# Optimization experiments

Hardware: AMD Instinct MI355X
Metric: run time of the kernel (lower is better)

The kernel has to match this reference:

```python
import jax, jax.numpy as jnp
import numpy as np

EMBED_DIM = 128
NUM_SYMBOLS = 200000
PAD_IDX = NUM_SYMBOLS
K_NEIGHBORS = 10
PROCESS_STEPS = 4
D_MODEL = 2 * EMBED_DIM   # 256
D_INNER = 2 * D_MODEL     # 512
LSTM_HID = 2 * D_MODEL    # 512
B, F_SUP, MAX_K = 4096, 5, 64


def setup_inputs() -> dict:
    key = jax.random.key(0)
    ks = jax.random.split(key, 40)
    f = lambda i, shape, s=0.05: jax.random.normal(ks[i], shape, jnp.float32) * s
    inp = {}
    inp['query'] = jax.random.randint(ks[0], (B, 2), 0, NUM_SYMBOLS)
    inp['support'] = jax.random.randint(ks[1], (F_SUP, 2), 0, NUM_SYMBOLS)
    inp['q_l1'] = jax.random.randint(ks[2], (B, MAX_K, 2), 0, NUM_SYMBOLS + 1)
    inp['q_deg_l'] = jax.random.randint(ks[3], (B,), 0, 100)
    inp['q_r1'] = jax.random.randint(ks[4], (B, MAX_K, 2), 0, NUM_SYMBOLS + 1)
    inp['q_deg_r'] = jax.random.randint(ks[5], (B,), 0, 100)
    inp['s_l1'] = jax.random.randint(ks[6], (F_SUP, MAX_K, 2), 0, NUM_SYMBOLS + 1)
    inp['s_deg_l'] = jax.random.randint(ks[7], (F_SUP,), 0, 100)
    inp['s_r1'] = jax.random.randint(ks[8], (F_SUP, MAX_K, 2), 0, NUM_SYMBOLS + 1)
    inp['s_deg_r'] = jax.random.randint(ks[9], (F_SUP,), 0, 100)
    # learned parameters
    inp['symbol_emb'] = f(10, (NUM_SYMBOLS + 1, EMBED_DIM), 0.1).at[PAD_IDX].set(0.0)
    inp['gcn_w_w'] = f(11, (EMBED_DIM, 2 * EMBED_DIM))
    inp['gcn_w_b'] = jnp.zeros((EMBED_DIM,), jnp.float32)
    inp['gcn_b'] = jnp.zeros((EMBED_DIM,), jnp.float32)
    inp['g1_w'] = f(12, (EMBED_DIM // 2, EMBED_DIM))
    inp['g1_b'] = jnp.zeros((EMBED_DIM // 2,), jnp.float32)
    inp['ln1_g'] = jnp.ones((EMBED_DIM // 2,), jnp.float32)
    inp['ln1_b'] = jnp.zeros((EMBED_DIM // 2,), jnp.float32)
    inp['g2_w'] = f(13, (1, EMBED_DIM // 2))
    inp['g2_b'] = jnp.zeros((1,), jnp.float32)
    inp['gate_temp'] = jnp.array(1.0, jnp.float32)
    inp['se_p1_w'] = f(14, (D_INNER, D_MODEL))
    inp['se_p1_b'] = jnp.zeros((D_INNER,), jnp.float32)
    inp['se_p2_w'] = f(15, (D_MODEL, D_INNER))
    inp['se_p2_b'] = jnp.zeros((D_MODEL,), jnp.float32)
    inp['se_ln_g'] = jnp.ones((D_MODEL,), jnp.float32)
    inp['se_ln_b'] = jnp.zeros((D_MODEL,), jnp.float32)
    inp['w_ih'] = f(16, (4 * LSTM_HID, D_MODEL))
    inp['w_hh'] = f(17, (4 * LSTM_HID, LSTM_HID))
    inp['b_ih'] = jnp.zeros((4 * LSTM_HID,), jnp.float32)
    inp['b_hh'] = jnp.zeros((4 * LSTM_HID,), jnp.float32)
    return inp


def _layernorm(x, g, b, eps=1e-5):
    m = jnp.mean(x, axis=-1, keepdims=True)
    v = jnp.var(x, axis=-1, keepdims=True)
    return (x - m) / jnp.sqrt(v + eps) * g + b


def _l2norm(x):
    return x / jnp.maximum(jnp.linalg.norm(x, axis=-1, keepdims=True), 1e-12)


def _neighbor_encoder(conn, deg, self_ids, p):
    emb = p['symbol_emb']
    rel, ent = conn[:, :, 0], conn[:, :, 1]
    rel_emb = emb[rel]            # [n, K, D] gather
    ent_emb = emb[ent]            # [n, K, D]
    self_emb = emb[self_ids]      # [n, D]
    sim = jnp.einsum('nd,nkd->nk', _l2norm(self_emb), _l2norm(ent_emb))
    is_pad = (rel == PAD_IDX).astype(jnp.float32)
    sim = sim - is_pad * 1e9
    k = min(K_NEIGHBORS, conn.shape[1])
    _, k_idx = jax.lax.top_k(sim, k)
    bidx = jnp.arange(conn.shape[0])[:, None]
    k_mask = jnp.zeros(sim.shape, jnp.float32).at[bidx, k_idx].set(1.0)[..., None]
    concat = jnp.concatenate([rel_emb, ent_emb], axis=-1)   # [n, K, 2D]
    proj = jax.nn.leaky_relu(concat @ p['gcn_w_w'].T + p['gcn_w_b'] + p['gcn_b'], 0.01)
    valid = (1.0 - is_pad[..., None]) * k_mask
    denom = jnp.maximum(jnp.sum(valid, axis=1), 1.0)
    agg = jnp.sum((proj * k_mask) * valid, axis=1) / denom   # [n, D]
    h = jax.nn.relu(_layernorm(agg @ p['g1_w'].T + p['g1_b'], p['ln1_g'], p['ln1_b']))
    logit = h @ p['g2_w'].T + p['g2_b']                      # [n, 1]
    temp = jnp.clip(p['gate_temp'], 0.1, 5.0)
    gate = jax.nn.sigmoid(logit / temp) * (deg > 0).astype(jnp.float32)[:, None]
    return jnp.tanh(self_emb + gate * agg)


def _support_encoder(x, p):
    h = jax.nn.relu(x @ p['se_p1_w'].T + p['se_p1_b'])
    h = h @ p['se_p2_w'].T + p['se_p2_b']
    return _layernorm(h + x, p['se_ln_g'], p['se_ln_b'])


def _query_encoder(support, query, p):
    n = query.shape[0]
    h_r0 = jnp.zeros((n, LSTM_HID), jnp.float32)
    c0 = jnp.zeros((n, LSTM_HID), jnp.float32)

    def step(carry, _):
        h_r, c = carry
        gates = query @ p['w_ih'].T + p['b_ih'] + h_r @ p['w_hh'].T + p['b_hh']
        i, f, g, o = jnp.split(gates, 4, axis=-1)
        c = jax.nn.sigmoid(f) * c + jax.nn.sigmoid(i) * jnp.tanh(g)
        h_ = jax.nn.sigmoid(o) * jnp.tanh(c)
        h = query + h_[:, :D_MODEL]
        attn = jax.nn.softmax(h @ support.T, axis=1)
        r = attn @ support
        return (jnp.concatenate([h, r], axis=-1), c), None

    (h_r, _), _ = jax.lax.scan(step, (h_r0, c0), None, length=PROCESS_STEPS)
    return h_r[:, :D_MODEL]


def reference(query, support, q_l1, q_deg_l, q_r1, q_deg_r, s_l1, s_deg_l, s_r1, s_deg_r,
              symbol_emb, gcn_w_w, gcn_w_b, gcn_b, g1_w, g1_b, ln1_g, ln1_b, g2_w, g2_b,
              gate_temp, se_p1_w, se_p1_b, se_p2_w, se_p2_b, se_ln_g, se_ln_b,
              w_ih, w_hh, b_ih, b_hh):
    p = dict(symbol_emb=symbol_emb, gcn_w_w=gcn_w_w, gcn_w_b=gcn_w_b, gcn_b=gcn_b,
             g1_w=g1_w, g1_b=g1_b, ln1_g=ln1_g, ln1_b=ln1_b, g2_w=g2_w, g2_b=g2_b,
             gate_temp=gate_temp, se_p1_w=se_p1_w, se_p1_b=se_p1_b, se_p2_w=se_p2_w,
             se_p2_b=se_p2_b, se_ln_g=se_ln_g, se_ln_b=se_ln_b,
             w_ih=w_ih, w_hh=w_hh, b_ih=b_ih, b_hh=b_hh)
    q_left = _neighbor_encoder(q_l1, q_deg_l, query[:, 0], p)
    q_right = _neighbor_encoder(q_r1, q_deg_r, query[:, 1], p)
    query_vec = jnp.concatenate([q_left, q_right], axis=-1)      # [B, 2D]
    s_left = _neighbor_encoder(s_l1, s_deg_l, support[:, 0], p)
    s_right = _neighbor_encoder(s_r1, s_deg_r, support[:, 1], p)
    support_vec = jnp.concatenate([s_left, s_right], axis=-1)    # [F, 2D]
    support_g = jnp.mean(_support_encoder(support_vec, p), axis=0, keepdims=True)  # [1, 2D]
    query_enc = _support_encoder(query_vec, p)                   # [B, 2D]
    query_g = _query_encoder(support_g, query_enc, p)            # [B, 2D]
    return jnp.sum(query_g * support_g, axis=1)                  # [B]
```

## Files before the change

kernel.cpp:

```cpp
#include <hip/hip_runtime.h>
#include <math.h>

#define BQ 4096
#define F_SUP 5
#define MAXK 64
#define ED 128
#define DM 256
#define DI 512
#define LH 512
#define NG 2048
#define PADX 200000
#define KNB 10
#define MROWS 82048
#define MREAL 82020
#define MQ 4224
#define EMB_ELEMS 25600128

typedef unsigned short u16;
typedef __attribute__((ext_vector_type(8))) short short8;
typedef __attribute__((ext_vector_type(4))) float floatx4;

__device__ __forceinline__ float sigf(float x) { return 1.0f / (1.0f + __expf(-x)); }
__device__ __forceinline__ float tanh_fast(float x) {
  float a = fabsf(x);
  float e = __expf(-2.0f * a);
  float t = (1.0f - e) / (1.0f + e);
  return copysignf(t, x);
}
__device__ __forceinline__ u16 f2bf(float f) {
  unsigned u = __float_as_uint(f);
  unsigned r = (u + 0x7FFFu + ((u >> 16) & 1u)) >> 16;
  return (u16)r;
}
__device__ __forceinline__ float bf2f(u16 u) {
  return __uint_as_float(((unsigned)u) << 16);
}
__device__ __forceinline__ void gl2lds16(const void* g, void* l) {
  __builtin_amdgcn_global_load_lds(
      (const __attribute__((address_space(1))) void*)g,
      (__attribute__((address_space(3))) void*)l, 16, 0, 0);
}

__global__ __launch_bounds__(256) void emb_cast_kernel(
    const float* __restrict__ emb, u16* __restrict__ embb)
{
  long i = ((long)blockIdx.x * 256 + threadIdx.x) * 8;
  if (i >= (long)EMB_ELEMS) return;
  float4 f0 = *(const float4*)(emb + i);
  float4 f1 = *(const float4*)(emb + i + 4);
  short8 s;
  s[0]=(short)f2bf(f0.x); s[1]=(short)f2bf(f0.y); s[2]=(short)f2bf(f0.z); s[3]=(short)f2bf(f0.w);
  s[4]=(short)f2bf(f1.x); s[5]=(short)f2bf(f1.y); s[6]=(short)f2bf(f1.z); s[7]=(short)f2bf(f1.w);
  *(short8*)(embb + i) = s;
}

__global__ __launch_bounds__(256) void nbr_simrank_kernel(
    const int* __restrict__ query, const int* __restrict__ support,
    const int* __restrict__ q_l1, const int* __restrict__ q_r1,
    const int* __restrict__ s_l1, const int* __restrict__ s_r1,
    const u16* __restrict__ embb, int* __restrict__ idxA, int* __restrict__ meta)
{
  __shared__ float sE[128];
  __shared__ float simS[64];
  __shared__ int relS[64], entS[64];
  int tid = threadIdx.x;
  int b = blockIdx.x;
  const int* conn; int self_id;
  if (b < BQ)              { int i = b;              conn = q_l1 + (long)i*(MAXK*2); self_id = query[2*i];   }
  else if (b < 2*BQ)       { int i = b - BQ;         conn = q_r1 + (long)i*(MAXK*2); self_id = query[2*i+1]; }
  else if (b < 2*BQ+F_SUP) { int i = b - 2*BQ;       conn = s_l1 + (long)i*(MAXK*2); self_id = support[2*i]; }
  else                     { int i = b - 2*BQ-F_SUP; conn = s_r1 + (long)i*(MAXK*2); self_id = support[2*i+1]; }

  int k = tid >> 2, part = tid & 3;
  int2 rc = *(const int2*)(conn + 2 * k);
  if (tid < 16) {
    short8 s = *(const short8*)(embb + (long)self_id * ED + tid * 8);
    #pragma unroll
    for (int j = 0; j < 8; ++j) sE[tid * 8 + j] = bf2f((u16)s[j]);
  }
  __syncthreads();

  const u16* er = embb + (long)rc.y * ED + part * 8;
  float dot = 0.f, sq = 0.f;
  #pragma unroll
  for (int i = 0; i < 4; ++i) {
    short8 e8 = *(const short8*)(er + i * 32);
    #pragma unroll
    for (int j = 0; j < 8; ++j) {
      float e = bf2f((u16)e8[j]);
      float s = sE[i * 32 + part * 8 + j];
      dot += e * s; sq += e * e;
    }
  }
  dot += __shfl_xor(dot, 1); dot += __shfl_xor(dot, 2);
  sq  += __shfl_xor(sq, 1);  sq  += __shfl_xor(sq, 2);
  if (part == 0) {
    float ne = fmaxf(sqrtf(sq), 1e-12f);
    float sim = dot / ne;
    if (rc.x == PADX) sim -= 1e9f;
    simS[k] = sim; relS[k] = rc.x; entS[k] = rc.y;
  }
  __syncthreads();

  if (tid < 64) {
    float my = simS[tid];
    int rank = 0;
    #pragma unroll
    for (int j = 0; j < 64; ++j) {
      float s = simS[j];
      rank += ((s > my) || (s == my && j < tid)) ? 1 : 0;
    }
    bool val = (rank < KNB) && (relS[tid] != PADX);
    unsigned long long vm = __ballot(val ? 1 : 0);
    int cnt = __popcll(vm);
    long base = (long)b * 10;
    if (val) {
      int pos = __popcll(vm & ((1ull << tid) - 1ull));
      int2 p; p.x = relS[tid]; p.y = entS[tid];
      *(int2*)(idxA + (base + pos) * 2) = p;
    }
    if (tid >= cnt && tid < KNB) {
      int2 pp; pp.x = PADX; pp.y = PADX;
      *(int2*)(idxA + (base + tid) * 2) = pp;
    }
    if (tid == 0) meta[b] = cnt;
  }
  if (b == 0 && tid >= 64 && tid < 64 + 2 * (MROWS - MREAL)) {
    idxA[(long)MREAL * 2 + (tid - 64)] = PADX;
  }
}

__global__ __launch_bounds__(256) void proj_gather_gemm(
    const int* __restrict__ idxA, const u16* __restrict__ embb,
    const u16* __restrict__ W, u16* __restrict__ proj)
{
  __shared__ u16 As[128 * 32];
  __shared__ u16 Bs[128 * 32];
  __shared__ int idxS[256];
  int tid = threadIdx.x;
  int bm = blockIdx.x;
  idxS[tid] = idxA[bm * 256 + tid];
  int lane = tid & 63, wave = tid >> 6;
  int wm = (wave & 1) * 64, wn = (wave >> 1) * 64;
  int col = lane & 15, quad = lane >> 4;

  floatx4 acc[4][4];
  #pragma unroll
  for (int i = 0; i < 4; ++i)
    #pragma unroll
    for (int j = 0; j < 4; ++j) { floatx4 z = {0.f,0.f,0.f,0.f}; acc[i][j] = z; }
  __syncthreads();

  for (int k0 = 0; k0 < 256; k0 += 32) {
    int half = k0 >> 7, koff = k0 & 127;
    #pragma unroll
    for (int t = 0; t < 2; ++t) {
      int c = t * 256 + tid;
      int rb = c >> 2, o = c & 3;
      int og = o ^ (rb & 3);
      gl2lds16(W + (long)rb * 256 + k0 + og * 8, &Bs[(size_t)c * 8]);
      int id = idxS[rb * 2 + half];
      gl2lds16(embb + (long)id * ED + koff + og * 8, &As[(size_t)c * 8]);
    }
    __syncthreads();
    short8 af[4], bfr[4];
    #pragma unroll
    for (int i = 0; i < 4; ++i) {
      int ra = wm + i * 16 + col;
      af[i] = *(const short8*)&As[(size_t)(ra * 4 + (quad ^ (ra & 3))) * 8];
      int rb = wn + i * 16 + col;
      bfr[i] = *(const short8*)&Bs[(size_t)(rb * 4 + (quad ^ (rb & 3))) * 8];
    }
    #pragma unroll
    for (int i = 0; i < 4; ++i)
      #pragma unroll
      for (int j = 0; j < 4; ++j)
        acc[i][j] = __builtin_amdgcn_mfma_f32_16x16x32_bf16(af[i], bfr[j], acc[i][j], 0, 0, 0);
    __syncthreads();
  }
  int gm0 = bm * 128 + wm + quad * 4;
  int gn0 = wn + col;
  #pragma unroll
  for (int i = 0; i < 4; ++i)
    #pragma unroll
    for (int j = 0; j < 4; ++j)
      #pragma unroll
      for (int rr = 0; rr < 4; ++rr)
        proj[(long)(gm0 + i * 16 + rr) * 128 + gn0 + j * 16] = f2bf(acc[i][j][rr]);
}

__global__ __launch_bounds__(128) void nbr_post_kernel(
    const int* __restrict__ query, const int* __restrict__ support,
    const int* __restrict__ q_deg_l, const int* __restrict__ q_deg_r,
    const int* __restrict__ s_deg_l, const int* __restrict__ s_deg_r,
    const float* __restrict__ emb,
    const u16* __restrict__ proj, const int* __restrict__ meta,
    const float* __restrict__ gcn_w_b, const float* __restrict__ gcn_b,
    const float* __restrict__ g1_w, const float* __restrict__ g1_b,
    const float* __restrict__ ln1_g, const float* __restrict__ ln1_b,
    const float* __restrict__ g2_w, const float* __restrict__ g2_b,
    const float* __restrict__ gate_temp,
    float* __restrict__ qv, u16* __restrict__ qv_bf)
{
  __shared__ __align__(16) float aggS[128];
  __shared__ float sEs[128];
  __shared__ float gateS;
  int tid = threadIdx.x, b = blockIdx.x;
  int deg, self_id, row, colb;
  if (b < BQ)              { int i = b;              deg = q_deg_l[i]; self_id = query[2*i];     row = i;        colb = 0;  }
  else if (b < 2*BQ)       { int i = b - BQ;         deg = q_deg_r[i]; self_id = query[2*i+1];   row = i;        colb = ED; }
  else if (b < 2*BQ+F_SUP) { int i = b - 2*BQ;       deg = s_deg_l[i]; self_id = support[2*i];   row = BQ + i;   colb = 0;  }
  else                     { int i = b - 2*BQ-F_SUP; deg = s_deg_r[i]; self_id = support[2*i+1]; row = BQ + i;   colb = ED; }
  float* outp = qv + (long)row * DM + colb;
  u16*  outpb = qv_bf + (long)row * DM + colb;

  int cnt = meta[b];
  float denom = fmaxf((float)cnt, 1.0f);
  float bsum = gcn_w_b[tid] + gcn_b[tid];
  float agg = 0.f;
  long pbase = (long)b * 10;
  for (int kk = 0; kk < cnt; ++kk) {
    float z = bf2f(proj[(pbase + kk) * 128 + tid]) + bsum;
    z = (z >= 0.f) ? z : 0.01f * z;
    agg += z;
  }
  agg /= denom;
  aggS[tid] = agg;
  sEs[tid] = emb[(long)self_id * ED + tid];
  __syncthreads();

  if (tid < 64) {
    int e = tid;
    const float4* g1r = (const float4*)(g1_w + e * ED);
    float y = g1_b[e];
    #pragma unroll 8
    for (int j = 0; j < 32; ++j) {
      float4 w = g1r[j];
      float4 a = *(const float4*)&aggS[j * 4];
      y += w.x*a.x + w.y*a.y + w.z*a.z + w.w*a.w;
    }
    float s = y;
    #pragma unroll
    for (int off = 1; off < 64; off <<= 1) s += __shfl_xor(s, off);
    float mean = s * (1.0f / 64.0f);
    float dv = y - mean;
    float s2 = dv * dv;
    #pragma unroll
    for (int off = 1; off < 64; off <<= 1) s2 += __shfl_xor(s2, off);
    float var = s2 * (1.0f / 64.0f);
    float hv = dv / sqrtf(var + 1e-5f) * ln1_g[e] + ln1_b[e];
    hv = fmaxf(hv, 0.f);
    float lp = hv * g2_w[e];
    #pragma unroll
    for (int off = 1; off < 64; off <<= 1) lp += __shfl_xor(lp, off);
    if (e == 0) {
      float logit = lp + g2_b[0];
      float temp = fminf(fmaxf(gate_temp[0], 0.1f), 5.0f);
      float gate = 1.0f / (1.0f + expf(-logit / temp));
      if (deg <= 0) gate = 0.f;
      gateS = gate;
    }
  }
  __syncthreads();
  float o = tanhf(sEs[tid] + gateS * aggS[tid]);
  outp[tid] = o;
  outpb[tid] = f2bf(o);
}

__global__ __launch_bounds__(256) void mfma_gemm(
    const u16* __restrict__ A, int lda,
    const u16* __restrict__ W, int ldw,
    int N, int K,
    float* __restrict__ Cout, u16* __restrict__ Cbf,
    const float* __restrict__ bias0,
    const u16* __restrict__ gqin,
    u16* __restrict__ gqout,
    int relu, int lstm_mode,
    float* __restrict__ cstate, const float* __restrict__ qe,
    u16* __restrict__ hbf)
{
  __shared__ u16 As[128 * 32];
  __shared__ u16 Bs[128 * 32];
  int tid = threadIdx.x;
  int nb = N >> 7;
  int bn = blockIdx.x % nb, bm = blockIdx.x / nb;
  int lane = tid & 63, wave = tid >> 6;
  int wm = (wave & 1) * 64, wn = (wave >> 1) * 64;
  int col = lane & 15, quad = lane >> 4;

  u16 gqa[64]; float cpv[16]; float qev[16]; float scv[4];
  int u = 0; long fb = 0;
  if (lstm_mode) {
    u = bn * 32 + (wave >> 1) * 16 + col;
    fb = ((long)blockIdx.x * 4 + wave) * 64 + lane;
    #pragma unroll
    for (int j = 0; j < 4; ++j)
      scv[j] = bias0[bn * 128 + (wave >> 1) * 64 + j * 16 + col];
    if (lstm_mode == 1) {
      const short8* gp = (const short8*)(gqin + fb * 64);
      #pragma unroll
      for (int t = 0; t < 8; ++t) *(short8*)&gqa[t * 8] = gp[t];
      const float4* cp = (const float4*)(cstate + fb * 16);
      #pragma unroll
      for (int t = 0; t < 4; ++t) *(float4*)&cpv[t * 4] = cp[t];
    }
    if (u < DM) {
      #pragma unroll
      for (int i = 0; i < 4; ++i)
        #pragma unroll
        for (int r = 0; r < 4; ++r) {
          int m = bm * 128 + (wave & 1) * 64 + i * 16 + quad * 4 + r;
          qev[i * 4 + r] = qe[(long)m * DM + u];
        }
    }
  }

  floatx4 acc[4][4];
  #pragma unroll
  for (int i = 0; i < 4; ++i)
    #pragma unroll
    for (int j = 0; j < 4; ++j) { floatx4 z = {0.f,0.f,0.f,0.f}; acc[i][j] = z; }

  for (int k0 = 0; k0 < K; k0 += 32) {
    #pragma unroll
    for (int t = 0; t < 2; ++t) {
      int c = t * 256 + tid;
      int r = c >> 2, o = c & 3;
      int og = o ^ (r & 3);
      gl2lds16(A + (long)(bm * 128 + r) * lda + k0 + og * 8, &As[(size_t)c * 8]);
      gl2lds16(W + (long)(bn * 128 + r) * ldw + k0 + og * 8, &Bs[(size_t)c * 8]);
    }
    __syncthreads();
    short8 af[4], bfr[4];
    #pragma unroll
    for (int i = 0; i < 4; ++i) {
      int ra = wm + i * 16 + col;
      af[i] = *(const short8*)&As[(size_t)(ra * 4 + (quad ^ (ra & 3))) * 8];
      int rb = wn + i * 16 + col;
      bfr[i] = *(const short8*)&Bs[(size_t)(rb * 4 + (quad ^ (rb & 3))) * 8];
    }
    #pragma unroll
    for (int i = 0; i < 4; ++i)
      #pragma unroll
      for (int j = 0; j < 4; ++j)
        acc[i][j] = __builtin_amdgcn_mfma_f32_16x16x32_bf16(af[i], bfr[j], acc[i][j], 0, 0, 0);
    __syncthreads();
  }

  if (lstm_mode) {
    float cnew[16];
    #pragma unroll
    for (int i = 0; i < 4; ++i) {
      #pragma unroll
      for (int r = 0; r < 4; ++r) {
        float gI = acc[i][0][r] + scv[0];
        float gF = acc[i][1][r] + scv[1];
        float gG = acc[i][2][r] + scv[2];
        float gO = acc[i][3][r] + scv[3];
        if (lstm_mode == 1) {
          gI += bf2f(gqa[(i * 4 + 0) * 4 + r]);
          gF += bf2f(gqa[(i * 4 + 1) * 4 + r]);
          gG += bf2f(gqa[(i * 4 + 2) * 4 + r]);
          gO += bf2f(gqa[(i * 4 + 3) * 4 + r]);
        }
        float cp = (lstm_mode == 2) ? 0.f : cpv[i * 4 + r];
        float cn = sigf(gF) * cp + sigf(gI) * tanh_fast(gG);
        cnew[i * 4 + r] = cn;
        if (u < DM) {
          int m = bm * 128 + (wave & 1) * 64 + i * 16 + quad * 4 + r;
          hbf[(long)m * DM + u] = f2bf(qev[i * 4 + r] + sigf(gO) * tanh_fast(cn));
        }
      }
    }
    {
      float4* cp = (float4*)(cstate + fb * 16);
      #pragma unroll
      for (int t = 0; t < 4; ++t) cp[t] = *(float4*)&cnew[t * 4];
    }
    if (lstm_mode == 2) {
      u16 ga[64];
      #pragma unroll
      for (int i = 0; i < 4; ++i)
        #pragma unroll
        for (int j = 0; j < 4; ++j)
          #pragma unroll
          for (int r = 0; r < 4; ++r)
            ga[(i * 4 + j) * 4 + r] = f2bf(acc[i][j][r] + scv[j]);
      short8* gp = (short8*)(gqout + fb * 64);
      #pragma unroll
      for (int t = 0; t < 8; ++t) gp[t] = *(short8*)&ga[t * 8];
    }
  } else {
    int gm0 = bm * 128 + wm + quad * 4;
    int gn0 = bn * 128 + wn + col;
    #pragma unroll
    for (int i = 0; i < 4; ++i) {
      #pragma unroll
      for (int j = 0; j < 4; ++j) {
        int n = gn0 + j * 16;
        #pragma unroll
        for (int r = 0; r < 4; ++r) {
          int m = gm0 + i * 16 + r;
          float v = acc[i][j][r];
          if (bias0) v += bias0[n];
          if (relu) v = fmaxf(v, 0.f);
          if (Cout) Cout[(long)m * N + n] = v;
          if (Cbf)  Cbf[(long)m * N + n] = f2bf(v);
        }
      }
    }
  }
}

__global__ void prep_cast(
    const float* __restrict__ p1, const float* __restrict__ p2,
    const float* __restrict__ gcnw, const float* __restrict__ wih,
    const float* __restrict__ whh, const float* __restrict__ bih,
    const float* __restrict__ bhh,
    u16* __restrict__ p1b, u16* __restrict__ p2b, u16* __restrict__ gcnb,
    u16* __restrict__ wihb, u16* __restrict__ whhb, float* __restrict__ bihh)
{
  int gid = blockIdx.x * 256 + threadIdx.x;
  if (gid < 131072) { p1b[gid] = f2bf(p1[gid]); }
  else if (gid < 262144) { int i = gid - 131072; p2b[i] = f2bf(p2[i]); }
  else if (gid < 294912) { int i = gid - 262144; gcnb[i] = f2bf(gcnw[i]); }
  else if (gid < 819200) {
    int i = gid - 294912; int p = i >> 8, k = i & 255;
    int g = (p >> 4) & 3, uu = (p >> 7) * 32 + ((p >> 6) & 1) * 16 + (p & 15);
    int n = g * 512 + uu;
    wihb[i] = f2bf(wih[(long)n * DM + k]);
  } else if (gid < 1343488) {
    int i = gid - 819200; int p = i >> 8, k = i & 255;
    int g = (p >> 4) & 3, uu = (p >> 7) * 32 + ((p >> 6) & 1) * 16 + (p & 15);
    int n = g * 512 + uu;
    whhb[i] = f2bf(whh[(long)n * LH + k]);
  } else if (gid < 1345536) {
    int p = gid - 1343488;
    int g = (p >> 4) & 3, uu = (p >> 7) * 32 + ((p >> 6) & 1) * 16 + (p & 15);
    int n = g * 512 + uu;
    bihh[p] = bih[n] + bhh[n];
  }
}

__global__ __launch_bounds__(256) void ln_residual_kernel(
    const float* __restrict__ h2buf, const float* __restrict__ xbuf,
    const float* __restrict__ lng, const float* __restrict__ lnb,
    float* __restrict__ out, u16* __restrict__ outb)
{
  __shared__ float red[4];
  int r = blockIdx.x, tid = threadIdx.x;
  float v = h2buf[(long)r * DM + tid] + xbuf[(long)r * DM + tid];
  float s = v;
  #pragma unroll
  for (int off = 1; off < 64; off <<= 1) s += __shfl_xor(s, off);
  if ((tid & 63) == 0) red[tid >> 6] = s;
  __syncthreads();
  float mean = (red[0] + red[1] + red[2] + red[3]) * (1.0f / 256.0f);
  __syncthreads();
  float dv = v - mean;
  float s2 = dv * dv;
  #pragma unroll
  for (int off = 1; off < 64; off <<= 1) s2 += __shfl_xor(s2, off);
  if ((tid & 63) == 0) red[tid >> 6] = s2;
  __syncthreads();
  float var = (red[0] + red[1] + red[2] + red[3]) * (1.0f / 256.0f);
  float o = dv / sqrtf(var + 1e-5f) * lng[tid] + lnb[tid];
  out[(long)r * DM + tid] = o;
  outb[(long)r * DM + tid] = f2bf(o);
}

__global__ __launch_bounds__(256) void scorr_kernel(
    const float* __restrict__ qe, const float* __restrict__ whh,
    float* __restrict__ sg, float* __restrict__ s_corr_perm)
{
  __shared__ float sgS[DM];
  int tid = threadIdx.x;
  {
    float v = 0.f;
    #pragma unroll
    for (int r = 0; r < F_SUP; ++r) v += qe[(long)(BQ + r) * DM + tid];
    v *= (1.0f / (float)F_SUP);
    sgS[tid] = v;
    if (blockIdx.x == 0) sg[tid] = v;
  }
  __syncthreads();
  int wave = tid >> 6, lane = tid & 63;
  int n = blockIdx.x * 4 + wave;
  float4 w = *(const float4*)(whh + (long)n * LH + DM + lane * 4);
  float4 s = *(const float4*)&sgS[lane * 4];
  float d = w.x*s.x + w.y*s.y + w.z*s.z + w.w*s.w;
  #pragma unroll
  for (int off = 1; off < 64; off <<= 1) d += __shfl_xor(d, off);
  if (lane == 0) {
    int g = n >> 9, uu = n & 511;
    int p = (uu >> 5) * 128 + ((uu >> 4) & 1) * 64 + g * 16 + (uu & 15);
    s_corr_perm[p] = d;
  }
}

__global__ __launch_bounds__(256) void final_dot_kernel(
    const u16* __restrict__ h, const float* __restrict__ sg, float* __restrict__ out)
{
  __shared__ float red[4];
  int m = blockIdx.x, tid = threadIdx.x;
  float v = bf2f(h[(long)m * DM + tid]) * sg[tid];
  #pragma unroll
  for (int off = 1; off < 64; off <<= 1) v += __shfl_xor(v, off);
  if ((tid & 63) == 0) red[tid >> 6] = v;
  __syncthreads();
  if (tid == 0) out[m] = red[0] + red[1] + red[2] + red[3];
}

extern "C" void kernel_launch(void* const* d_in, const int* in_sizes, int n_in,
                              void* d_out, int out_size, void* d_ws, size_t ws_size,
                              hipStream_t stream)
{
  const int*   query    = (const int*)  d_in[0];
  const int*   support  = (const int*)  d_in[1];
  const int*   q_l1     = (const int*)  d_in[2];
  const int*   q_deg_l  = (const int*)  d_in[3];
  const int*   q_r1     = (const int*)  d_in[4];
  const int*   q_deg_r  = (const int*)  d_in[5];
  const int*   s_l1     = (const int*)  d_in[6];
  const int*   s_deg_l  = (const int*)  d_in[7];
  const int*   s_r1     = (const int*)  d_in[8];
  const int*   s_deg_r  = (const int*)  d_in[9];
  const float* symbol_emb = (const float*)d_in[10];
  const float* gcn_w_w  = (const float*)d_in[11];
  const float* gcn_w_b  = (const float*)d_in[12];
  const float* gcn_b    = (const float*)d_in[13];
  const float* g1_w     = (const float*)d_in[14];
  const float* g1_b     = (const float*)d_in[15];
  const float* ln1_g    = (const float*)d_in[16];
  const float* ln1_b    = (const float*)d_in[17];
  const float* g2_w     = (const float*)d_in[18];
  const float* g2_b     = (const float*)d_in[19];
  const float* gate_temp= (const float*)d_in[20];
  const float* se_p1_w  = (const float*)d_in[21];
  const float* se_p1_b  = (const float*)d_in[22];
  const float* se_p2_w  = (const float*)d_in[23];
  const float* se_p2_b  = (const float*)d_in[24];
  const float* se_ln_g  = (const float*)d_in[25];
  const float* se_ln_b  = (const float*)d_in[26];
  const float* w_ih     = (const float*)d_in[27];
  const float* w_hh     = (const float*)d_in[28];
  const float* b_ih     = (const float*)d_in[29];
  const float* b_hh     = (const float*)d_in[30];

  float* ws = (float*)d_ws;
  size_t off = 0;
  float* projF   = ws + off; off += (size_t)MROWS * 128 / 2;
  float* idxF    = ws + off; off += (size_t)MROWS * 2;
  float* qv      = ws + off; off += (size_t)MQ * DM;
  float* qe      = ws + off; off += (size_t)MQ * DM;
  float* qv_bfF  = ws + off; off += (size_t)MQ * DM / 2;
  float* qe_bfF  = ws + off; off += (size_t)MQ * DM / 2;
  float* h1bF    = ws + off; off += (size_t)MQ * DI / 2;
  float* H2      = ws + off; off += (size_t)MQ * DM;
  float* gqbF    = ws + off; off += (size_t)BQ * NG / 2;
  float* cstate  = ws + off; off += (size_t)BQ * LH;
  float* hbf0F   = ws + off; off += (size_t)BQ * DM / 2;
  float* hbf1F   = ws + off; off += (size_t)BQ * DM / 2;
  float* p1bF    = ws + off; off += 131072 / 2;
  float* p2bF    = ws + off; off += 131072 / 2;
  float* gcnbF   = ws + off; off += 32768 / 2;
  float* wihbF   = ws + off; off += 524288 / 2;
  float* whhbF   = ws + off; off += 524288 / 2;
  float* bihh    = ws + off; off += 2048;
  float* sg      = ws + off; off += 256;
  float* s_corr  = ws + off; off += 2048;
  float* metaF   = ws + off; off += 8448;
  float* embbF   = ws + off; off += (size_t)EMB_ELEMS / 2;

  u16* proj   = (u16*)projF;
  int* idxA   = (int*)idxF;
  u16* qv_bf  = (u16*)qv_bfF;
  u16* qe_bf  = (u16*)qe_bfF;
  u16* H1_bf  = (u16*)h1bF;
  u16* gq_fr  = (u16*)gqbF;
  u16* hbf0   = (u16*)hbf0F;
  u16* hbf1   = (u16*)hbf1F;
  u16* p1b    = (u16*)p1bF;
  u16* p2b    = (u16*)p2bF;
  u16* gcnb   = (u16*)gcnbF;
  u16* wihb   = (u16*)wihbF;
  u16* whhb   = (u16*)whhbF;
  int* meta   = (int*)metaF;
  u16* embb   = (u16*)embbF;

  prep_cast<<<5256, 256, 0, stream>>>(se_p1_w, se_p2_w, gcn_w_w, w_ih, w_hh, b_ih, b_hh,
                                      p1b, p2b, gcnb, wihb, whhb, bihh);
  emb_cast_kernel<<<(EMB_ELEMS / 8 + 255) / 256, 256, 0, stream>>>(symbol_emb, embb);

  nbr_simrank_kernel<<<2 * BQ + 2 * F_SUP, 256, 0, stream>>>(
      query, support, q_l1, q_r1, s_l1, s_r1, embb, idxA, meta);

  proj_gather_gemm<<<MROWS / 128, 256, 0, stream>>>(idxA, embb, gcnb, proj);

  nbr_post_kernel<<<2 * BQ + 2 * F_SUP, 128, 0, stream>>>(
      query, support, q_deg_l, q_deg_r, s_deg_l, s_deg_r, symbol_emb,
      proj, meta, gcn_w_b, gcn_b, g1_w, g1_b, ln1_g, ln1_b, g2_w, g2_b, gate_temp,
      qv, qv_bf);

  mfma_gemm<<<(MQ / 128) * (DI / 128), 256, 0, stream>>>(qv_bf, 256, p1b, 256, DI, 256,
      nullptr, H1_bf, se_p1_b, nullptr, nullptr, 1, 0, nullptr, nullptr, nullptr);
  mfma_gemm<<<(MQ / 128) * (DM / 128), 256, 0, stream>>>(H1_bf, 512, p2b, 512, DM, 512,
      H2, nullptr, se_p2_b, nullptr, nullptr, 0, 0, nullptr, nullptr, nullptr);
  ln_residual_kernel<<<BQ + F_SUP, 256, 0, stream>>>(H2, qv, se_ln_g, se_ln_b, qe, qe_bf);

  scorr_kernel<<<512, 256, 0, stream>>>(qe, w_hh, sg, s_corr);

  mfma_gemm<<<(BQ / 128) * (NG / 128), 256, 0, stream>>>(qe_bf, 256, wihb, 256, NG, 256,
      nullptr, nullptr, bihh, nullptr, gq_fr, 0, 2, cstate, qe, hbf0);

  mfma_gemm<<<(BQ / 128) * (NG / 128), 256, 0, stream>>>(hbf0, 256, whhb, 256, NG, 256,
      nullptr, nullptr, s_corr, gq_fr, nullptr, 0, 1, cstate, qe, hbf1);
  mfma_gemm<<<(BQ / 128) * (NG / 128), 256, 0, stream>>>(hbf1, 256, whhb, 256, NG, 256,
      nullptr, nullptr, s_corr, gq_fr, nullptr, 0, 1, cstate, qe, hbf0);
  mfma_gemm<<<(BQ / 128) * (NG / 128), 256, 0, stream>>>(hbf0, 256, whhb, 256, NG, 256,
      nullptr, nullptr, s_corr, gq_fr, nullptr, 0, 1, cstate, qe, hbf1);

  final_dot_kernel<<<BQ, 256, 0, stream>>>(hbf1, sg, (float*)d_out);
}
```

Measured before the change: 426.5 us.

## Merge prep casts, fold scorr into LSTM GEMM, fuse final dot into last step

Result: slower. 443.7 us (+4.0%).

```diff
diff --git a/kernel.cpp b/kernel.cpp
--- a/kernel.cpp
+++ b/kernel.cpp
@@ -15,6 +15,7 @@
 #define MREAL 82020
 #define MQ 4224
 #define EMB_ELEMS 25600128
+#define NEMB8 3200016
 
 typedef unsigned short u16;
 typedef __attribute__((ext_vector_type(8))) short short8;
@@ -41,17 +42,49 @@
       (__attribute__((address_space(3))) void*)l, 16, 0, 0);
 }
 
-__global__ __launch_bounds__(256) void emb_cast_kernel(
-    const float* __restrict__ emb, u16* __restrict__ embb)
+__global__ __launch_bounds__(256) void prep_all(
+    const float* __restrict__ emb, u16* __restrict__ embb,
+    const float* __restrict__ p1, const float* __restrict__ p2,
+    const float* __restrict__ gcnw, const float* __restrict__ wih,
+    const float* __restrict__ whh, const float* __restrict__ bih,
+    const float* __restrict__ bhh,
+    u16* __restrict__ p1b, u16* __restrict__ p2b, u16* __restrict__ gcnb,
+    u16* __restrict__ wihb, u16* __restrict__ whhb, float* __restrict__ bihh,
+    float* __restrict__ outz)
 {
-  long i = ((long)blockIdx.x * 256 + threadIdx.x) * 8;
-  if (i >= (long)EMB_ELEMS) return;
-  float4 f0 = *(const float4*)(emb + i);
-  float4 f1 = *(const float4*)(emb + i + 4);
-  short8 s;
-  s[0]=(short)f2bf(f0.x); s[1]=(short)f2bf(f0.y); s[2]=(short)f2bf(f0.z); s[3]=(short)f2bf(f0.w);
-  s[4]=(short)f2bf(f1.x); s[5]=(short)f2bf(f1.y); s[6]=(short)f2bf(f1.z); s[7]=(short)f2bf(f1.w);
-  *(short8*)(embb + i) = s;
+  long gid = (long)blockIdx.x * 256 + threadIdx.x;
+  if (gid < (long)NEMB8) {
+    long i = gid * 8;
+    float4 f0 = *(const float4*)(emb + i);
+    float4 f1 = *(const float4*)(emb + i + 4);
+    short8 s;
+    s[0]=(short)f2bf(f0.x); s[1]=(short)f2bf(f0.y); s[2]=(short)f2bf(f0.z); s[3]=(short)f2bf(f0.w);
+    s[4]=(short)f2bf(f1.x); s[5]=(short)f2bf(f1.y); s[6]=(short)f2bf(f1.z); s[7]=(short)f2bf(f1.w);
+    *(short8*)(embb + i) = s;
+    return;
+  }
+  int g2 = (int)(gid - NEMB8);
+  if (g2 < 131072) { p1b[g2] = f2bf(p1[g2]); }
+  else if (g2 < 262144) { int i = g2 - 131072; p2b[i] = f2bf(p2[i]); }
+  else if (g2 < 294912) { int i = g2 - 262144; gcnb[i] = f2bf(gcnw[i]); }
+  else if (g2 < 819200) {
+    int i = g2 - 294912; int p = i >> 8, k = i & 255;
+    int g = (p >> 4) & 3, uu = (p >> 7) * 32 + ((p >> 6) & 1) * 16 + (p & 15);
+    int n = g * 512 + uu;
+    wihb[i] = f2bf(wih[(long)n * DM + k]);
+  } else if (g2 < 1343488) {
+    int i = g2 - 819200; int p = i >> 8, k = i & 255;
+    int g = (p >> 4) & 3, uu = (p >> 7) * 32 + ((p >> 6) & 1) * 16 + (p & 15);
+    int n = g * 512 + uu;
+    whhb[i] = f2bf(whh[(long)n * LH + k]);
+  } else if (g2 < 1345536) {
+    int p = g2 - 1343488;
+    int g = (p >> 4) & 3, uu = (p >> 7) * 32 + ((p >> 6) & 1) * 16 + (p & 15);
+    int n = g * 512 + uu;
+    bihh[p] = bih[n] + bhh[n];
+  } else if (g2 < 1345536 + BQ) {
+    outz[g2 - 1345536] = 0.f;
+  }
 }
 
 __global__ __launch_bounds__(256) void nbr_simrank_kernel(
@@ -277,11 +310,39 @@
     u16* __restrict__ gqout,
     int relu, int lstm_mode,
     float* __restrict__ cstate, const float* __restrict__ qe,
-    u16* __restrict__ hbf)
+    u16* __restrict__ hbf,
+    const float* __restrict__ sgv, float* __restrict__ dotv,
+    const float* __restrict__ whh_f, float* __restrict__ sgo, float* __restrict__ sco)
 {
   __shared__ u16 As[128 * 32];
   __shared__ u16 Bs[128 * 32];
   int tid = threadIdx.x;
+
+  if (lstm_mode == 2 && whh_f && blockIdx.x >= gridDim.x - 512) {
+    int sc = blockIdx.x - (gridDim.x - 512);
+    float* sgS = (float*)As;
+    float v = 0.f;
+    #pragma unroll
+    for (int r = 0; r < F_SUP; ++r) v += qe[(long)(BQ + r) * DM + tid];
+    v *= (1.0f / (float)F_SUP);
+    sgS[tid] = v;
+    if (sc == 0) sgo[tid] = v;
+    __syncthreads();
+    int wv = tid >> 6, lane = tid & 63;
+    int n = sc * 4 + wv;
+    float4 w = *(const float4*)(whh_f + (long)n * LH + DM + lane * 4);
+    float4 s = *(const float4*)&sgS[lane * 4];
+    float d = w.x*s.x + w.y*s.y + w.z*s.z + w.w*s.w;
+    #pragma unroll
+    for (int off = 1; off < 64; off <<= 1) d += __shfl_xor(d, off);
+    if (lane == 0) {
+      int g = n >> 9, uu = n & 511;
+      int p = (uu >> 5) * 128 + ((uu >> 4) & 1) * 64 + g * 16 + (uu & 15);
+      sco[p] = d;
+    }
+    return;
+  }
+
   int nb = N >> 7;
   int bn = blockIdx.x % nb, bm = blockIdx.x / nb;
   int lane = tid & 63, wave = tid >> 6;
@@ -292,11 +353,11 @@
   int u = 0; long fb = 0;
   if (lstm_mode) {
     u = bn * 32 + (wave >> 1) * 16 + col;
-    fb = ((long)blockIdx.x * 4 + wave) * 64 + lane;
+    fb = ((long)(bm * (NG >> 7) + bn) * 4 + wave) * 64 + lane;
     #pragma unroll
     for (int j = 0; j < 4; ++j)
       scv[j] = bias0[bn * 128 + (wave >> 1) * 64 + j * 16 + col];
-    if (lstm_mode == 1) {
+    if (lstm_mode != 2) {
       const short8* gp = (const short8*)(gqin + fb * 64);
       #pragma unroll
       for (int t = 0; t < 8; ++t) *(short8*)&gqa[t * 8] = gp[t];
@@ -347,7 +408,28 @@
     __syncthreads();
   }
 
-  if (lstm_mode) {
+  if (lstm_mode == 3) {
+    float sgu = sgv[u];
+    #pragma unroll
+    for (int i = 0; i < 4; ++i) {
+      #pragma unroll
+      for (int r = 0; r < 4; ++r) {
+        float gI = acc[i][0][r] + scv[0] + bf2f(gqa[(i * 4 + 0) * 4 + r]);
+        float gF = acc[i][1][r] + scv[1] + bf2f(gqa[(i * 4 + 1) * 4 + r]);
+        float gG = acc[i][2][r] + scv[2] + bf2f(gqa[(i * 4 + 2) * 4 + r]);
+        float gO = acc[i][3][r] + scv[3] + bf2f(gqa[(i * 4 + 3) * 4 + r]);
+        float cn = sigf(gF) * cpv[i * 4 + r] + sigf(gI) * tanh_fast(gG);
+        float hv = qev[i * 4 + r] + sigf(gO) * tanh_fast(cn);
+        float p = hv * sgu;
+        p += __shfl_xor(p, 1); p += __shfl_xor(p, 2);
+        p += __shfl_xor(p, 4); p += __shfl_xor(p, 8);
+        if (col == 0) {
+          int m = bm * 128 + (wave & 1) * 64 + i * 16 + quad * 4 + r;
+          atomicAdd(&dotv[m], p);
+        }
+      }
+    }
+  } else if (lstm_mode) {
     float cnew[16];
     #pragma unroll
     for (int i = 0; i < 4; ++i) {
@@ -412,36 +494,6 @@
   }
 }
 
-__global__ void prep_cast(
-    const float* __restrict__ p1, const float* __restrict__ p2,
-    const float* __restrict__ gcnw, const float* __restrict__ wih,
-    const float* __restrict__ whh, const float* __restrict__ bih,
-    const float* __restrict__ bhh,
-    u16* __restrict__ p1b, u16* __restrict__ p2b, u16* __restrict__ gcnb,
-    u16* __restrict__ wihb, u16* __restrict__ whhb, float* __restrict__ bihh)
-{
-  int gid = blockIdx.x * 256 + threadIdx.x;
-  if (gid < 131072) { p1b[gid] = f2bf(p1[gid]); }
-  else if (gid < 262144) { int i = gid - 131072; p2b[i] = f2bf(p2[i]); }
-  else if (gid < 294912) { int i = gid - 262144; gcnb[i] = f2bf(gcnw[i]); }
-  else if (gid < 819200) {
-    int i = gid - 294912; int p = i >> 8, k = i & 255;
-    int g = (p >> 4) & 3, uu = (p >> 7) * 32 + ((p >> 6) & 1) * 16 + (p & 15);
-    int n = g * 512 + uu;
-    wihb[i] = f2bf(wih[(long)n * DM + k]);
-  } else if (gid < 1343488) {
-    int i = gid - 819200; int p = i >> 8, k = i & 255;
-    int g = (p >> 4) & 3, uu = (p >> 7) * 32 + ((p >> 6) & 1) * 16 + (p & 15);
-    int n = g * 512 + uu;
-    whhb[i] = f2bf(whh[(long)n * LH + k]);
-  } else if (gid < 1345536) {
-    int p = gid - 1343488;
-    int g = (p >> 4) & 3, uu = (p >> 7) * 32 + ((p >> 6) & 1) * 16 + (p & 15);
-    int n = g * 512 + uu;
-    bihh[p] = bih[n] + bhh[n];
-  }
-}
-
 __global__ __launch_bounds__(256) void ln_residual_kernel(
     const float* __restrict__ h2buf, const float* __restrict__ xbuf,
     const float* __restrict__ lng, const float* __restrict__ lnb,
@@ -467,48 +519,6 @@
   float o = dv / sqrtf(var + 1e-5f) * lng[tid] + lnb[tid];
   out[(long)r * DM + tid] = o;
   outb[(long)r * DM + tid] = f2bf(o);
-}
-
-__global__ __launch_bounds__(256) void scorr_kernel(
-    const float* __restrict__ qe, const float* __restrict__ whh,
-    float* __restrict__ sg, float* __restrict__ s_corr_perm)
-{
-  __shared__ float sgS[DM];
-  int tid = threadIdx.x;
-  {
-    float v = 0.f;
-    #pragma unroll
-    for (int r = 0; r < F_SUP; ++r) v += qe[(long)(BQ + r) * DM + tid];
-    v *= (1.0f / (float)F_SUP);
-    sgS[tid] = v;
-    if (blockIdx.x == 0) sg[tid] = v;
-  }
-  __syncthreads();
-  int wave = tid >> 6, lane = tid & 63;
-  int n = blockIdx.x * 4 + wave;
-  float4 w = *(const float4*)(whh + (long)n * LH + DM + lane * 4);
-  float4 s = *(const float4*)&sgS[lane * 4];
-  float d = w.x*s.x + w.y*s.y + w.z*s.z + w.w*s.w;
-  #pragma unroll
-  for (int off = 1; off < 64; off <<= 1) d += __shfl_xor(d, off);
-  if (lane == 0) {
-    int g = n >> 9, uu = n & 511;
-    int p = (uu >> 5) * 128 + ((uu >> 4) & 1) * 64 + g * 16 + (uu & 15);
-    s_corr_perm[p] = d;
-  }
-}
-
-__global__ __launch_bounds__(256) void final_dot_kernel(
-    const u16* __restrict__ h, const float* __restrict__ sg, float* __restrict__ out)
-{
-  __shared__ float red[4];
-  int m = blockIdx.x, tid = threadIdx.x;
-  float v = bf2f(h[(long)m * DM + tid]) * sg[tid];
-  #pragma unroll
-  for (int off = 1; off < 64; off <<= 1) v += __shfl_xor(v, off);
-  if ((tid & 63) == 0) red[tid >> 6] = v;
-  __syncthreads();
-  if (tid == 0) out[m] = red[0] + red[1] + red[2] + red[3];
 }
 
 extern "C" void kernel_launch(void* const* d_in, const int* in_sizes, int n_in,
@@ -588,9 +598,13 @@
   int* meta   = (int*)metaF;
   u16* embb   = (u16*)embbF;
 
-  prep_cast<<<5256, 256, 0, stream>>>(se_p1_w, se_p2_w, gcn_w_w, w_ih, w_hh, b_ih, b_hh,
-                                      p1b, p2b, gcnb, wihb, whhb, bihh);
-  emb_cast_kernel<<<(EMB_ELEMS / 8 + 255) / 256, 256, 0, stream>>>(symbol_emb, embb);
+  {
+    long total = (long)NEMB8 + 1345536 + BQ;
+    int blocks = (int)((total + 255) / 256);
+    prep_all<<<blocks, 256, 0, stream>>>(symbol_emb, embb,
+        se_p1_w, se_p2_w, gcn_w_w, w_ih, w_hh, b_ih, b_hh,
+        p1b, p2b, gcnb, wihb, whhb, bihh, (float*)d_out);
+  }
 
   nbr_simrank_kernel<<<2 * BQ + 2 * F_SUP, 256, 0, stream>>>(
       query, support, q_l1, q_r1, s_l1, s_r1, embb, idxA, meta);
@@ -603,22 +617,25 @@
       qv, qv_bf);
 
   mfma_gemm<<<(MQ / 128) * (DI / 128), 256, 0, stream>>>(qv_bf, 256, p1b, 256, DI, 256,
-      nullptr, H1_bf, se_p1_b, nullptr, nullptr, 1, 0, nullptr, nullptr, nullptr);
+      nullptr, H1_bf, se_p1_b, nullptr, nullptr, 1, 0, nullptr, nullptr, nullptr,
+      nullptr, nullptr, nullptr, nullptr, nullptr);
   mfma_gemm<<<(MQ / 128) * (DM / 128), 256, 0, stream>>>(H1_bf, 512, p2b, 512, DM, 512,
-      H2, nullptr, se_p2_b, nullptr, nullptr, 0, 0, nullptr, nullptr, nullptr);
+      H2, nullptr, se_p2_b, nullptr, nullptr, 0, 0, nullptr, nullptr, nullptr,
+      nullptr, nullptr, nullptr, nullptr, nullptr);
   ln_residual_kernel<<<BQ + F_SUP, 256, 0, stream>>>(H2, qv, se_ln_g, se_ln_b, qe, qe_bf);
 
-  scorr_kernel<<<512, 256, 0, stream>>>(qe, w_hh, sg, s_corr);
-
-  mfma_gemm<<<(BQ / 128) * (NG / 128), 256, 0, stream>>>(qe_bf, 256, wihb, 256, NG, 256,
-      nullptr, nullptr, bihh, nullptr, gq_fr, 0, 2, cstate, qe, hbf0);
+  mfma_gemm<<<(BQ / 128) * (NG / 128) + 512, 256, 0, stream>>>(qe_bf, 256, wihb, 256, NG, 256,
+      nullptr, nullptr, bihh, nullptr, gq_fr, 0, 2, cstate, qe, hbf0,
+      nullptr, nullptr, w_hh, sg, s_corr);
 
   mfma_gemm<<<(BQ / 128) * (NG / 128), 256, 0, stream>>>(hbf0, 256, whhb, 256, NG, 256,
-      nullptr, nullptr, s_corr, gq_fr, nullptr, 0, 1, cstate, qe, hbf1);
+      nullptr, nullptr, s_corr, gq_fr, nullptr, 0, 1, cstate, qe, hbf1,
+      nullptr, nullptr, nullptr, nullptr, nullptr);
   mfma_gemm<<<(BQ / 128) * (NG / 128), 256, 0, stream>>>(hbf1, 256, whhb, 256, NG, 256,
-      nullptr, nullptr, s_corr, gq_fr, nullptr, 0, 1, cstate, qe, hbf0);
-  mfma_gemm<<<(BQ / 128) * (NG / 128), 256, 0, stream>>>(hbf0, 256, whhb, 256, NG, 256,
-      nullptr, nullptr, s_corr, gq_fr, nullptr, 0, 1, cstate, qe, hbf1);
-
-  final_dot_kernel<<<BQ, 256, 0, stream>>>(hbf1, sg, (float*)d_out);
-}
+      nullptr, nullptr, s_corr, gq_fr, nullptr, 0, 1, cstate, qe, hbf0,
+      nullptr, nullptr, nullptr, nullptr, nullptr);
+
+  mfma_gemm<<<(BQ / 128) * (1024 / 128), 256, 0, stream>>>(hbf0, 256, whhb, 256, 1024, 256,
+      nullptr, nullptr, s_corr, gq_fr, nullptr, 0, 3, cstate, qe, nullptr,
+      sg, (float*)d_out, nullptr, nullptr, nullptr);
+}
```
